# Optimization experiments

Hardware: AMD Instinct MI355X
Metric: run time of the kernel (lower is better)

## Reference

```python
import jax, jax.numpy as jnp
import numpy as np

# Model dims / constants (from par in init_kwargs)
B, N_IN, NN = 128, 1024, 512
DT, TAU_M, V_TH = 0.05, 10.0, 2.0
ALPHA = 1.0 - DT / TAU_M  # leak factor, 0.995


def setup_inputs() -> dict:
    key = jax.random.key(0)
    k1, k2, k3, k4 = jax.random.split(key, 4)
    x = jax.random.normal(k1, (B, N_IN, NN), dtype=jnp.float32)          # input traces per neuron
    w = jax.random.normal(k2, (N_IN, NN), dtype=jnp.float32) / np.sqrt(N_IN)  # init.normal_(std=1/sqrt(n_in))
    v = jax.random.normal(k3, (B, NN), dtype=jnp.float32)                # membrane potential state
    z = (jax.random.uniform(k4, (B, NN)) < 0.1).astype(jnp.float32)      # previous spikes (0/1)
    return {"x": x, "w": w, "v": v, "z": z}


def reference(x, w, v, z):
    # LIF membrane update, vectorized over the batch (original uses a per-batch Python loop):
    #   v[b] = alpha*v[b] + sum_i x[b,i,:]*w[i,:] - v_th*z[b].detach()
    v_new = ALPHA * v + jnp.sum(x * w[None, :, :], axis=1) - V_TH * jax.lax.stop_gradient(z)
    # threshold nonlinearity -> output spikes
    z_new = (v_new - V_TH > 0).astype(v_new.dtype)
    return v_new, z_new
```

## Files before the change

### kernel.cpp

```cpp
#include <hip/hip_runtime.h>


typedef float f32x4 __attribute__((ext_vector_type(4)));

constexpr int B    = 128;
constexpr int N_IN = 1024;
constexpr int NN   = 512;
constexpr int NN4  = NN / 4;
constexpr int IG   = 8;
constexpr int IPG  = N_IN / IG;
constexpr int IPT  = IPG / 4;
constexpr float ALPHA = 1.0f - 0.05f / 10.0f;
constexpr float V_TH  = 2.0f;

__global__ __launch_bounds__(256) void lif_partial(
    const f32x4* __restrict__ x4,
    const f32x4* __restrict__ w4,
    f32x4* __restrict__ part)
{
    const int t    = threadIdx.x;
    const int g    = t & 63;
    const int c    = t >> 6;
    const int sub  = blockIdx.x & 15;
    const int bq   = blockIdx.x >> 4;
    const int slab = sub & 1;
    const int ig   = sub >> 1;

    const int b0  = bq * 4;
    const int col = slab * 64 + g;
    const int i0  = ig * IPG + c * IPT;

    const size_t bstride = (size_t)N_IN * NN4;
    const f32x4* __restrict__ xp0 = x4 + (size_t)b0 * bstride + (size_t)i0 * NN4 + col;
    const f32x4* __restrict__ xp1 = xp0 + bstride;
    const f32x4* __restrict__ xp2 = xp1 + bstride;
    const f32x4* __restrict__ xp3 = xp2 + bstride;
    const f32x4* __restrict__ wp  = w4 + (size_t)i0 * NN4 + col;

    f32x4 a0 = {0.f, 0.f, 0.f, 0.f};
    f32x4 a1 = {0.f, 0.f, 0.f, 0.f};
    f32x4 a2 = {0.f, 0.f, 0.f, 0.f};
    f32x4 a3 = {0.f, 0.f, 0.f, 0.f};
    #pragma unroll 4
    for (int ii = 0; ii < IPT; ++ii) {
        const size_t off = (size_t)ii * NN4;
        f32x4 wv  = wp[off];
        f32x4 xv0 = __builtin_nontemporal_load(&xp0[off]);
        f32x4 xv1 = __builtin_nontemporal_load(&xp1[off]);
        f32x4 xv2 = __builtin_nontemporal_load(&xp2[off]);
        f32x4 xv3 = __builtin_nontemporal_load(&xp3[off]);
        a0 += xv0 * wv;
        a1 += xv1 * wv;
        a2 += xv2 * wv;
        a3 += xv3 * wv;
    }

    __shared__ f32x4 red[4][256];
    red[0][t] = a0; red[1][t] = a1; red[2][t] = a2; red[3][t] = a3;
    __syncthreads();
    if (t < 128) {
        #pragma unroll
        for (int k = 0; k < 4; ++k) red[k][t] += red[k][t + 128];
    }
    __syncthreads();
    if (t < 64) {
        #pragma unroll
        for (int k = 0; k < 4; ++k) {
            f32x4 s = red[k][t] + red[k][t + 64];
            part[(((size_t)ig * B + b0 + k) * 2 + slab) * 64 + t] = s;
        }
    }
}

__global__ __launch_bounds__(256) void lif_finalize(
    const f32x4* __restrict__ part,
    const f32x4* __restrict__ v4,
    const f32x4* __restrict__ z4,
    f32x4* __restrict__ vout4,
    f32x4* __restrict__ zout4)
{
    const int idx = blockIdx.x * 256 + threadIdx.x;
    if (idx >= B * NN4) return;
    f32x4 s = part[idx];
    #pragma unroll
    for (int igr = 1; igr < IG; ++igr)
        s += part[(size_t)igr * B * NN4 + idx];
    f32x4 vv = v4[idx];
    f32x4 zz = z4[idx];
    f32x4 vn = ALPHA * vv + s - V_TH * zz;
    vout4[idx] = vn;
    f32x4 zn;
    zn.x = (vn.x - V_TH > 0.f) ? 1.f : 0.f;
    zn.y = (vn.y - V_TH > 0.f) ? 1.f : 0.f;
    zn.z = (vn.z - V_TH > 0.f) ? 1.f : 0.f;
    zn.w = (vn.w - V_TH > 0.f) ? 1.f : 0.f;
    zout4[idx] = zn;
}

extern "C" void kernel_launch(void* const* d_in, const int* in_sizes, int n_in,
                              void* d_out, int out_size, void* d_ws, size_t ws_size,
                              hipStream_t stream) {
    const f32x4* x = (const f32x4*)d_in[0];
    const f32x4* w = (const f32x4*)d_in[1];
    const f32x4* v = (const f32x4*)d_in[2];
    const f32x4* z = (const f32x4*)d_in[3];
    f32x4* vout = (f32x4*)d_out;
    f32x4* zout = vout + (size_t)B * NN4;
    f32x4* part = (f32x4*)d_ws;

    lif_partial<<<dim3(32 * 16), dim3(256), 0, stream>>>(x, w, part);
    lif_finalize<<<dim3((B * NN4 + 255) / 256), dim3(256), 0, stream>>>(
        part, v, z, vout, zout);
}
```

Baseline: 54.96 us.

## Repartition LIF reduction: 2 batches per block, 16 input groups, full-row columns

Work is split differently across blocks. Each block now handles 2 batch rows instead of 4, covers all 128 vector columns instead of a 64-column slab, and uses 16 input groups of 64 rows instead of 8. This doubles the grid to 1024 blocks, so more waves are in flight to hide latency on the memory-bound read of x, and the shared-memory reduction drops to a single step. In exchange there are twice as many partial sums for the finalize kernel to read, and each w load is reused across only 2 batches instead of 4.

```diff
diff --git a/kernel.cpp b/kernel.cpp
--- a/kernel.cpp
+++ b/kernel.cpp
@@ -7,9 +7,9 @@
 constexpr int N_IN = 1024;
 constexpr int NN   = 512;
 constexpr int NN4  = NN / 4;
-constexpr int IG   = 8;
+constexpr int IG   = 16;
 constexpr int IPG  = N_IN / IG;
-constexpr int IPT  = IPG / 4;
+constexpr int IPT  = IPG / 2;
 constexpr float ALPHA = 1.0f - 0.05f / 10.0f;
 constexpr float V_TH  = 2.0f;
 
@@ -18,57 +18,43 @@
     const f32x4* __restrict__ w4,
     f32x4* __restrict__ part)
 {
-    const int t    = threadIdx.x;
-    const int g    = t & 63;
-    const int c    = t >> 6;
-    const int sub  = blockIdx.x & 15;
-    const int bq   = blockIdx.x >> 4;
-    const int slab = sub & 1;
-    const int ig   = sub >> 1;
+    const int t  = threadIdx.x;
+    const int g  = t & 127;
+    const int c  = t >> 7;
+    const int ig = blockIdx.x & 15;
+    const int bp = blockIdx.x >> 4;
 
-    const int b0  = bq * 4;
-    const int col = slab * 64 + g;
-    const int i0  = ig * IPG + c * IPT;
+    const int b0 = bp * 2;
+    const int i0 = ig * IPG + c * IPT;
 
     const size_t bstride = (size_t)N_IN * NN4;
-    const f32x4* __restrict__ xp0 = x4 + (size_t)b0 * bstride + (size_t)i0 * NN4 + col;
+    const f32x4* __restrict__ xp0 = x4 + (size_t)b0 * bstride + (size_t)i0 * NN4 + g;
     const f32x4* __restrict__ xp1 = xp0 + bstride;
-    const f32x4* __restrict__ xp2 = xp1 + bstride;
-    const f32x4* __restrict__ xp3 = xp2 + bstride;
-    const f32x4* __restrict__ wp  = w4 + (size_t)i0 * NN4 + col;
+    const f32x4* __restrict__ wp  = w4 + (size_t)i0 * NN4 + g;
 
     f32x4 a0 = {0.f, 0.f, 0.f, 0.f};
     f32x4 a1 = {0.f, 0.f, 0.f, 0.f};
-    f32x4 a2 = {0.f, 0.f, 0.f, 0.f};
-    f32x4 a3 = {0.f, 0.f, 0.f, 0.f};
     #pragma unroll 4
     for (int ii = 0; ii < IPT; ++ii) {
         const size_t off = (size_t)ii * NN4;
         f32x4 wv  = wp[off];
         f32x4 xv0 = __builtin_nontemporal_load(&xp0[off]);
         f32x4 xv1 = __builtin_nontemporal_load(&xp1[off]);
-        f32x4 xv2 = __builtin_nontemporal_load(&xp2[off]);
-        f32x4 xv3 = __builtin_nontemporal_load(&xp3[off]);
         a0 += xv0 * wv;
         a1 += xv1 * wv;
-        a2 += xv2 * wv;
-        a3 += xv3 * wv;
     }
 
-    __shared__ f32x4 red[4][256];
-    red[0][t] = a0; red[1][t] = a1; red[2][t] = a2; red[3][t] = a3;
+    __shared__ f32x4 red0[256];
+    __shared__ f32x4 red1[256];
+    red0[t] = a0;
+    red1[t] = a1;
     __syncthreads();
+
     if (t < 128) {
-        #pragma unroll
-        for (int k = 0; k < 4; ++k) red[k][t] += red[k][t + 128];
-    }
-    __syncthreads();
-    if (t < 64) {
-        #pragma unroll
-        for (int k = 0; k < 4; ++k) {
-            f32x4 s = red[k][t] + red[k][t + 64];
-            part[(((size_t)ig * B + b0 + k) * 2 + slab) * 64 + t] = s;
-        }
+        f32x4 s0 = red0[t] + red0[t + 128];
+        f32x4 s1 = red1[t] + red1[t + 128];
+        part[((size_t)ig * B + b0)     * NN4 + t] = s0;
+        part[((size_t)ig * B + b0 + 1) * NN4 + t] = s1;
     }
 }
 
@@ -108,7 +94,7 @@
     f32x4* zout = vout + (size_t)B * NN4;
     f32x4* part = (f32x4*)d_ws;
 
-    lif_partial<<<dim3(32 * 16), dim3(256), 0, stream>>>(x, w, part);
+    lif_partial<<<dim3(64 * IG), dim3(256), 0, stream>>>(x, w, part);
     lif_finalize<<<dim3((B * NN4 + 255) / 256), dim3(256), 0, stream>>>(
         part, v, z, vout, zout);
 }
```

After: 51.47 us. -6.3%, faster.
